# Performance work log

Hardware: AMD Instinct MI355X
Metric: run time of the kernel (lower is better)

The kernel has to match this reference:

```python
import jax, jax.numpy as jnp
import numpy as np


def setup_inputs() -> dict:
    key = jax.random.key(0)
    kx, ky = jax.random.split(key)
    x = jax.random.normal(kx, (16, 4096, 3), dtype=jnp.float32)
    y = jax.random.normal(ky, (16, 4096, 3), dtype=jnp.float32)
    return {"x": x, "y": y}


def reference(x, y):
    # avoiding the O(b*N*M*d) difference tensor of the naive expansion.
    x2 = jnp.sum(x * x, axis=-1)                  # (b, N)
    y2 = jnp.sum(y * y, axis=-1)                  # (b, M)
    xy = jnp.einsum('bnd,bmd->bnm', x, y)         # (b, N, M)
    dist = x2[:, :, None] + y2[:, None, :] - 2.0 * xy
    min_d = jnp.min(dist, axis=2)                 # top-1 smallest over M -> (b, N)
    chamfer = jnp.sum(min_d, axis=1) / x.shape[1] # (b,)
    return jnp.sum(chamfer)
```

## Files before the change

kernel.cpp:

```cpp
#include <hip/hip_runtime.h>


constexpr int NPTS    = 4096;
constexpr int NBATCH  = 16;
constexpr int BLOCK   = 256;
constexpr int XPT     = 8;
constexpr int XCHUNK  = BLOCK * XPT;
constexpr int YTILE   = 256;
constexpr int NXC     = NPTS / XCHUNK;
constexpr int NYC     = NPTS / YTILE;

__global__ __launch_bounds__(BLOCK) void chamfer_min_kernel(
    const float* __restrict__ x, const float* __restrict__ y,
    unsigned int* __restrict__ ws_min)
{
    __shared__ float4 sy[YTILE];

    const int b      = blockIdx.x >> 5;
    const int xchunk = (blockIdx.x >> 4) & (NXC - 1);
    const int ychunk = blockIdx.x & (NYC - 1);

    {
        const float* yp = y + ((size_t)b * NPTS + ychunk * YTILE + threadIdx.x) * 3;
        const float y0 = yp[0], y1 = yp[1], y2 = yp[2];
        sy[threadIdx.x] = make_float4(
            2.0f * y0, 2.0f * y1, 2.0f * y2,
            fmaf(y2, y2, fmaf(y1, y1, y0 * y0)));
    }

    const int xbase = xchunk * XCHUNK + threadIdx.x * XPT;
    const float4* xp4 = (const float4*)(x + ((size_t)b * NPTS + xbase) * 3);
    const float4 a0 = xp4[0], a1 = xp4[1], a2 = xp4[2];
    const float4 a3 = xp4[3], a4 = xp4[4], a5 = xp4[5];
    const float xa[XPT][3] = {
        {a0.x, a0.y, a0.z}, {a0.w, a1.x, a1.y},
        {a1.z, a1.w, a2.x}, {a2.y, a2.z, a2.w},
        {a3.x, a3.y, a3.z}, {a3.w, a4.x, a4.y},
        {a4.z, a4.w, a5.x}, {a5.y, a5.z, a5.w}};

    float x2s[XPT];
    #pragma unroll
    for (int i = 0; i < XPT; ++i)
        x2s[i] = fmaf(xa[i][2], xa[i][2],
                 fmaf(xa[i][1], xa[i][1], xa[i][0] * xa[i][0]));

    __syncthreads();

    float m[XPT];
    #pragma unroll
    for (int i = 0; i < XPT; ++i) m[i] = 3.4e38f;

    #pragma unroll 2
    for (int j = 0; j < YTILE; j += 2) {
        const float4 Y0 = sy[j];
        const float4 Y1 = sy[j + 1];
        #pragma unroll
        for (int i = 0; i < XPT; ++i) {
            const float t0 = fmaf(-xa[i][0], Y0.x,
                             fmaf(-xa[i][1], Y0.y,
                             fmaf(-xa[i][2], Y0.z, Y0.w)));
            const float t1 = fmaf(-xa[i][0], Y1.x,
                             fmaf(-xa[i][1], Y1.y,
                             fmaf(-xa[i][2], Y1.z, Y1.w)));
            m[i] = fminf(m[i], fminf(t0, t1));
        }
    }

    unsigned int* wm = ws_min + (size_t)b * NPTS + xbase;
    #pragma unroll
    for (int i = 0; i < XPT; ++i) {
        const float d = fmaxf(x2s[i] + m[i], 0.0f);
        atomicMin(&wm[i], __float_as_uint(d));
    }
}

__global__ __launch_bounds__(BLOCK) void chamfer_sum_kernel(
    const unsigned int* __restrict__ ws_min, float* __restrict__ out)
{
    __shared__ float swsum[BLOCK / 64];
    const int total = NBATCH * NPTS;
    float s = 0.f;
    for (int i = blockIdx.x * BLOCK + threadIdx.x; i < total;
         i += gridDim.x * BLOCK)
        s += __uint_as_float(ws_min[i]);

    for (int off = 32; off > 0; off >>= 1)
        s += __shfl_down(s, off, 64);
    const int wave = threadIdx.x >> 6;
    if ((threadIdx.x & 63) == 0) swsum[wave] = s;
    __syncthreads();
    if (threadIdx.x == 0) {
        float t = 0.f;
        #pragma unroll
        for (int w = 0; w < BLOCK / 64; ++w) t += swsum[w];
        atomicAdd(out, t * (1.0f / NPTS));
    }
}

extern "C" void kernel_launch(void* const* d_in, const int* in_sizes, int n_in,
                              void* d_out, int out_size, void* d_ws, size_t ws_size,
                              hipStream_t stream) {
    const float* x = (const float*)d_in[0];
    const float* y = (const float*)d_in[1];
    float* out = (float*)d_out;
    unsigned int* ws_min = (unsigned int*)d_ws;

    hipMemsetAsync(ws_min, 0xFF, (size_t)NBATCH * NPTS * sizeof(unsigned int), stream);
    hipMemsetAsync(out, 0, sizeof(float), stream);

    const int grid1 = NBATCH * NXC * NYC;
    chamfer_min_kernel<<<grid1, BLOCK, 0, stream>>>(x, y, ws_min);
    chamfer_sum_kernel<<<64, BLOCK, 0, stream>>>(ws_min, out);
}
```

Baseline: 98.15 us.

## Replace atomicMin partial minima with per-ychunk workspace and separate reduce

```diff
diff --git a/kernel.cpp b/kernel.cpp
--- a/kernel.cpp
+++ b/kernel.cpp
@@ -1,31 +1,31 @@
 #include <hip/hip_runtime.h>
 
 
-constexpr int NPTS    = 4096;
-constexpr int NBATCH  = 16;
-constexpr int BLOCK   = 256;
-constexpr int XPT     = 8;
-constexpr int XCHUNK  = BLOCK * XPT;
-constexpr int YTILE   = 256;
-constexpr int NXC     = NPTS / XCHUNK;
-constexpr int NYC     = NPTS / YTILE;
-
-__global__ __launch_bounds__(BLOCK) void chamfer_min_kernel(
+constexpr int NPTS   = 4096;
+constexpr int NBATCH = 16;
+constexpr int BLOCK  = 256;
+constexpr int XPT    = 8;
+constexpr int XCHUNK = BLOCK * XPT;
+constexpr int NXC    = NPTS / XCHUNK;
+
+
+template <int NYC>
+__global__ __launch_bounds__(BLOCK, 4) void chamfer_part_kernel(
     const float* __restrict__ x, const float* __restrict__ y,
-    unsigned int* __restrict__ ws_min)
-{
+    float* __restrict__ ws)
+{
+    constexpr int YTILE = NPTS / NYC;
     __shared__ float4 sy[YTILE];
 
-    const int b      = blockIdx.x >> 5;
-    const int xchunk = (blockIdx.x >> 4) & (NXC - 1);
-    const int ychunk = blockIdx.x & (NYC - 1);
-
-    {
-        const float* yp = y + ((size_t)b * NPTS + ychunk * YTILE + threadIdx.x) * 3;
+    const int b      = blockIdx.x / (NXC * NYC);
+    const int xchunk = (blockIdx.x / NYC) % NXC;
+    const int ychunk = blockIdx.x % NYC;
+
+    for (int i = threadIdx.x; i < YTILE; i += BLOCK) {
+        const float* yp = y + ((size_t)b * NPTS + ychunk * YTILE + i) * 3;
         const float y0 = yp[0], y1 = yp[1], y2 = yp[2];
-        sy[threadIdx.x] = make_float4(
-            2.0f * y0, 2.0f * y1, 2.0f * y2,
-            fmaf(y2, y2, fmaf(y1, y1, y0 * y0)));
+        sy[i] = make_float4(2.0f * y0, 2.0f * y1, 2.0f * y2,
+                            fmaf(y2, y2, fmaf(y1, y1, y0 * y0)));
     }
 
     const int xbase = xchunk * XCHUNK + threadIdx.x * XPT;
@@ -51,7 +51,116 @@
     for (int i = 0; i < XPT; ++i) m[i] = 3.4e38f;
 
     #pragma unroll 2
-    for (int j = 0; j < YTILE; j += 2) {
+    for (int j = 0; j < YTILE; j += 4) {
+        const float4 Y0 = sy[j + 0];
+        const float4 Y1 = sy[j + 1];
+        const float4 Y2 = sy[j + 2];
+        const float4 Y3 = sy[j + 3];
+        #pragma unroll
+        for (int i = 0; i < XPT; ++i) {
+            const float t0 = fmaf(-xa[i][0], Y0.x,
+                             fmaf(-xa[i][1], Y0.y,
+                             fmaf(-xa[i][2], Y0.z, Y0.w)));
+            const float t1 = fmaf(-xa[i][0], Y1.x,
+                             fmaf(-xa[i][1], Y1.y,
+                             fmaf(-xa[i][2], Y1.z, Y1.w)));
+            const float t2 = fmaf(-xa[i][0], Y2.x,
+                             fmaf(-xa[i][1], Y2.y,
+                             fmaf(-xa[i][2], Y2.z, Y2.w)));
+            const float t3 = fmaf(-xa[i][0], Y3.x,
+                             fmaf(-xa[i][1], Y3.y,
+                             fmaf(-xa[i][2], Y3.z, Y3.w)));
+            m[i] = fminf(fminf(fminf(t0, t1), fminf(t2, t3)), m[i]);
+        }
+    }
+
+    float* wp = ws + ((size_t)b * NYC + ychunk) * NPTS + xbase;
+    const float d0 = fmaxf(x2s[0] + m[0], 0.0f);
+    const float d1 = fmaxf(x2s[1] + m[1], 0.0f);
+    const float d2 = fmaxf(x2s[2] + m[2], 0.0f);
+    const float d3 = fmaxf(x2s[3] + m[3], 0.0f);
+    const float d4 = fmaxf(x2s[4] + m[4], 0.0f);
+    const float d5 = fmaxf(x2s[5] + m[5], 0.0f);
+    const float d6 = fmaxf(x2s[6] + m[6], 0.0f);
+    const float d7 = fmaxf(x2s[7] + m[7], 0.0f);
+    ((float4*)wp)[0] = make_float4(d0, d1, d2, d3);
+    ((float4*)wp)[1] = make_float4(d4, d5, d6, d7);
+}
+
+
+template <int NYC>
+__global__ __launch_bounds__(BLOCK) void chamfer_reduce_kernel(
+    const float* __restrict__ ws, float* __restrict__ out)
+{
+    __shared__ float swsum[BLOCK / 64];
+    const int idx = blockIdx.x * BLOCK + threadIdx.x;
+    const int b   = idx / NPTS;
+    const int xp  = idx % NPTS;
+
+    float mn = 3.4e38f;
+    #pragma unroll
+    for (int yc = 0; yc < NYC; ++yc)
+        mn = fminf(mn, ws[((size_t)b * NYC + yc) * NPTS + xp]);
+
+    float s = mn;
+    for (int off = 32; off > 0; off >>= 1)
+        s += __shfl_down(s, off, 64);
+    const int wave = threadIdx.x >> 6;
+    if ((threadIdx.x & 63) == 0) swsum[wave] = s;
+    __syncthreads();
+    if (threadIdx.x == 0) {
+        float t = 0.f;
+        #pragma unroll
+        for (int w = 0; w < BLOCK / 64; ++w) t += swsum[w];
+        atomicAdd(out, t * (1.0f / NPTS));
+    }
+}
+
+
+constexpr int FB_YTILE = 256;
+constexpr int FB_NYC   = NPTS / FB_YTILE;
+
+__global__ __launch_bounds__(BLOCK) void chamfer_min_atomic_kernel(
+    const float* __restrict__ x, const float* __restrict__ y,
+    unsigned int* __restrict__ ws_min)
+{
+    __shared__ float4 sy[FB_YTILE];
+
+    const int b      = blockIdx.x / (NXC * FB_NYC);
+    const int xchunk = (blockIdx.x / FB_NYC) % NXC;
+    const int ychunk = blockIdx.x % FB_NYC;
+
+    {
+        const float* yp = y + ((size_t)b * NPTS + ychunk * FB_YTILE + threadIdx.x) * 3;
+        const float y0 = yp[0], y1 = yp[1], y2 = yp[2];
+        sy[threadIdx.x] = make_float4(2.0f * y0, 2.0f * y1, 2.0f * y2,
+                                      fmaf(y2, y2, fmaf(y1, y1, y0 * y0)));
+    }
+
+    const int xbase = xchunk * XCHUNK + threadIdx.x * XPT;
+    const float4* xp4 = (const float4*)(x + ((size_t)b * NPTS + xbase) * 3);
+    const float4 a0 = xp4[0], a1 = xp4[1], a2 = xp4[2];
+    const float4 a3 = xp4[3], a4 = xp4[4], a5 = xp4[5];
+    const float xa[XPT][3] = {
+        {a0.x, a0.y, a0.z}, {a0.w, a1.x, a1.y},
+        {a1.z, a1.w, a2.x}, {a2.y, a2.z, a2.w},
+        {a3.x, a3.y, a3.z}, {a3.w, a4.x, a4.y},
+        {a4.z, a4.w, a5.x}, {a5.y, a5.z, a5.w}};
+
+    float x2s[XPT];
+    #pragma unroll
+    for (int i = 0; i < XPT; ++i)
+        x2s[i] = fmaf(xa[i][2], xa[i][2],
+                 fmaf(xa[i][1], xa[i][1], xa[i][0] * xa[i][0]));
+
+    __syncthreads();
+
+    float m[XPT];
+    #pragma unroll
+    for (int i = 0; i < XPT; ++i) m[i] = 3.4e38f;
+
+    #pragma unroll 2
+    for (int j = 0; j < FB_YTILE; j += 2) {
         const float4 Y0 = sy[j];
         const float4 Y1 = sy[j + 1];
         #pragma unroll
@@ -97,18 +206,33 @@
     }
 }
 
+
 extern "C" void kernel_launch(void* const* d_in, const int* in_sizes, int n_in,
                               void* d_out, int out_size, void* d_ws, size_t ws_size,
                               hipStream_t stream) {
     const float* x = (const float*)d_in[0];
     const float* y = (const float*)d_in[1];
     float* out = (float*)d_out;
-    unsigned int* ws_min = (unsigned int*)d_ws;
-
-    hipMemsetAsync(ws_min, 0xFF, (size_t)NBATCH * NPTS * sizeof(unsigned int), stream);
+
     hipMemsetAsync(out, 0, sizeof(float), stream);
 
-    const int grid1 = NBATCH * NXC * NYC;
-    chamfer_min_kernel<<<grid1, BLOCK, 0, stream>>>(x, y, ws_min);
-    chamfer_sum_kernel<<<64, BLOCK, 0, stream>>>(ws_min, out);
-}
+    const size_t need32 = (size_t)NBATCH * 32 * NPTS * sizeof(float);
+    const size_t need16 = (size_t)NBATCH * 16 * NPTS * sizeof(float);
+
+    if (ws_size >= need32) {
+        float* ws = (float*)d_ws;
+        chamfer_part_kernel<32><<<NBATCH * NXC * 32, BLOCK, 0, stream>>>(x, y, ws);
+        chamfer_reduce_kernel<32><<<NBATCH * NPTS / BLOCK, BLOCK, 0, stream>>>(ws, out);
+    } else if (ws_size >= need16) {
+        float* ws = (float*)d_ws;
+        chamfer_part_kernel<16><<<NBATCH * NXC * 16, BLOCK, 0, stream>>>(x, y, ws);
+        chamfer_reduce_kernel<16><<<NBATCH * NPTS / BLOCK, BLOCK, 0, stream>>>(ws, out);
+    } else {
+        unsigned int* ws_min = (unsigned int*)d_ws;
+        hipMemsetAsync(ws_min, 0xFF, (size_t)NBATCH * NPTS * sizeof(unsigned int),
+                       stream);
+        chamfer_min_atomic_kernel<<<NBATCH * NXC * FB_NYC, BLOCK, 0, stream>>>(
+            x, y, ws_min);
+        chamfer_sum_kernel<<<64, BLOCK, 0, stream>>>(ws_min, out);
+    }
+}
```

Measured after the change: 85.31 us. 13.1% less time.
